# Optimization experiments

Hardware: AMD Instinct MI355X
Metric: run time of the kernel (lower is better)

## Reference

```python
import jax, jax.numpy as jnp
import numpy as np

E = 1024
B = 16384

def _ln(x, g, b, eps=1e-5):
    mu = jnp.mean(x, axis=-1, keepdims=True)
    var = jnp.mean(jnp.square(x - mu), axis=-1, keepdims=True)
    return (x - mu) * jax.lax.rsqrt(var + eps) * g + b

def setup_inputs() -> dict:
    key = jax.random.key(0)
    ks = jax.random.split(key, 16)
    s = 0.02
    return {
        'img_feat': jax.random.normal(ks[0], (B, E), jnp.float32),
        'txt_feat': jax.random.normal(ks[1], (B, E), jnp.float32),
        # MHA 1 (img queries txt): packed in_proj [3E, E] like torch
        'w_in1': jax.random.normal(ks[2], (3 * E, E), jnp.float32) * s,
        'b_in1': jnp.zeros((3 * E,), jnp.float32),
        'w_out1': jax.random.normal(ks[3], (E, E), jnp.float32) * s,
        'b_out1': jnp.zeros((E,), jnp.float32),
        # MHA 2 (txt queries img)
        'w_in2': jax.random.normal(ks[4], (3 * E, E), jnp.float32) * s,
        'b_in2': jnp.zeros((3 * E,), jnp.float32),
        'w_out2': jax.random.normal(ks[5], (E, E), jnp.float32) * s,
        'b_out2': jnp.zeros((E,), jnp.float32),
        # LayerNorms
        'g1': jnp.ones((E,), jnp.float32), 'be1': jnp.zeros((E,), jnp.float32),
        'g2': jnp.ones((E,), jnp.float32), 'be2': jnp.zeros((E,), jnp.float32),
        'g3': jnp.ones((E,), jnp.float32), 'be3': jnp.zeros((E,), jnp.float32),
        # FFN
        'w_ffn1': jax.random.normal(ks[6], (4 * E, E), jnp.float32) * s,
        'b_ffn1': jnp.zeros((4 * E,), jnp.float32),
        'w_ffn2': jax.random.normal(ks[7], (E, 4 * E), jnp.float32) * s,
        'b_ffn2': jnp.zeros((E,), jnp.float32),
    }

def _attn_seq1(q_in, kv_in, w_in, b_in, w_out, b_out):
    # seq_len==1 for both query and key: softmax over a single 1x1 score is
    # identically 1, so attention output == out_proj(v_proj(kv)). The q/k
    # projections cancel out exactly (same math as torch MHA in eval mode).
    wv = w_in[2 * E:]
    bv = b_in[2 * E:]
    v = kv_in @ wv.T + bv          # [B, E]
    return v @ w_out.T + b_out     # [B, E]

def reference(img_feat, txt_feat, w_in1, b_in1, w_out1, b_out1,
              w_in2, b_in2, w_out2, b_out2,
              g1, be1, g2, be2, g3, be3,
              w_ffn1, b_ffn1, w_ffn2, b_ffn2):
    img_att = _attn_seq1(img_feat, txt_feat, w_in1, b_in1, w_out1, b_out1)
    img = _ln(img_feat + img_att, g1, be1)
    txt_att = _attn_seq1(txt_feat, img, w_in2, b_in2, w_out2, b_out2)
    txt = _ln(txt_feat + txt_att, g2, be2)
    combined = img + txt
    h = jax.nn.gelu(combined @ w_ffn1.T + b_ffn1, approximate=False)
    ffn = h @ w_ffn2.T + b_ffn2
    return _ln(combined + ffn, g3, be3)
```

## Files before the change

kernel.cpp:

```cpp
#include <hip/hip_runtime.h>
#include <hip/hip_bf16.h>

typedef __bf16 bf16_t;
typedef __bf16 bf16x8 __attribute__((ext_vector_type(8)));
typedef __bf16 bf16x4 __attribute__((ext_vector_type(4)));
typedef float f32x4 __attribute__((ext_vector_type(4)));

static constexpr int E = 1024;
static constexpr int BROWS = 16384;
static constexpr size_t MB = 1ull << 20;

__device__ __forceinline__ float gelu_f(float x) {
  float t = __expf(-x * fmaf(0.0713548163f, x * x, 1.5957691216f));
  return x / (1.0f + t);
}

__global__ __launch_bounds__(256) void cvt_f32_bf16(const float* __restrict__ src,
                                                    bf16_t* __restrict__ dst, int n4) {
  int stride = gridDim.x * blockDim.x;
  for (int i = blockIdx.x * blockDim.x + threadIdx.x; i < n4; i += stride) {
    float4 v = reinterpret_cast<const float4*>(src)[i];
    bf16x4 o;
    o[0] = (bf16_t)v.x; o[1] = (bf16_t)v.y; o[2] = (bf16_t)v.z; o[3] = (bf16_t)v.w;
    reinterpret_cast<bf16x4*>(dst)[i] = o;
  }
}

__global__ __launch_bounds__(256) void cvt_transpose(const float* __restrict__ in,
                                                     bf16_t* __restrict__ out) {
  __shared__ float t[64][65];
  const int bx = blockIdx.x * 64, by = blockIdx.y * 64;
  const int tid = threadIdx.x;
  const int r = tid >> 2, c4 = (tid & 3) * 16;
#pragma unroll
  for (int j = 0; j < 4; ++j) {
    float4 v = *reinterpret_cast<const float4*>(&in[(long)(by + r) * E + bx + c4 + j * 4]);
    t[r][c4 + j * 4 + 0] = v.x;
    t[r][c4 + j * 4 + 1] = v.y;
    t[r][c4 + j * 4 + 2] = v.z;
    t[r][c4 + j * 4 + 3] = v.w;
  }
  __syncthreads();
#pragma unroll
  for (int j = 0; j < 16; j += 4) {
    bf16x4 o;
    o[0] = (bf16_t)t[c4 + j + 0][r];
    o[1] = (bf16_t)t[c4 + j + 1][r];
    o[2] = (bf16_t)t[c4 + j + 2][r];
    o[3] = (bf16_t)t[c4 + j + 3][r];
    *reinterpret_cast<bf16x4*>(&out[(long)(bx + r) * E + by + c4 + j]) = o;
  }
}

__global__ __launch_bounds__(256) void fuse_bias(const float* __restrict__ wo,
                                                 const float* __restrict__ bv,
                                                 const float* __restrict__ bo,
                                                 float* __restrict__ outb) {
  const int row = (blockIdx.x * 256 + threadIdx.x) >> 6;
  const int lane = threadIdx.x & 63;
  float s = 0.f;
  for (int k = lane; k < E; k += 64) s += wo[(long)row * E + k] * bv[k];
#pragma unroll
  for (int off = 32; off; off >>= 1) s += __shfl_down(s, off);
  if (lane == 0) outb[row] = s + bo[row];
}

__global__ __launch_bounds__(256) void gemm_bt_small(const bf16_t* __restrict__ A,
                                                     const bf16_t* __restrict__ Bw,
                                                     bf16_t* __restrict__ Cout, int K, int N,
                                                     int NBX) {
  const int nwg = gridDim.x;
  const int orig = blockIdx.x;
  const int q = nwg >> 3;
  const int wgid = (orig & 7) * q + (orig >> 3);
  const int bx = wgid % NBX;
  const int by = wgid / NBX;
  __shared__ bf16_t As[128 * 32];
  __shared__ bf16_t Bs[128 * 32];
  const int tid = threadIdx.x;
  const int lane = tid & 63;
  const int w = tid >> 6;
  const int wr = w >> 1, wc = w & 1;
  const long m0 = (long)by * 128;
  const long n0 = (long)bx * 128;
  const bf16_t* aSrc = A + (m0 + (tid >> 2)) * (long)K + (tid & 3) * 8;
  const bf16_t* bSrc = Bw + (n0 + (tid >> 2)) * (long)K + (tid & 3) * 8;
  f32x4 acc[4][4];
#pragma unroll
  for (int mi = 0; mi < 4; ++mi)
#pragma unroll
    for (int ni = 0; ni < 4; ++ni) acc[mi][ni] = {0.f, 0.f, 0.f, 0.f};
  const int nkt = K >> 5;
  for (int kt = 0; kt < nkt; ++kt) {
#pragma unroll
    for (int r = 0; r < 2; ++r) {
      __builtin_amdgcn_global_load_lds(
          (__attribute__((address_space(1))) void*)(aSrc + (long)r * 64 * K + kt * 32),
          (__attribute__((address_space(3))) void*)((char*)As + r * 4096 + w * 1024), 16, 0, 0);
      __builtin_amdgcn_global_load_lds(
          (__attribute__((address_space(1))) void*)(bSrc + (long)r * 64 * K + kt * 32),
          (__attribute__((address_space(3))) void*)((char*)Bs + r * 4096 + w * 1024), 16, 0, 0);
    }
    __syncthreads();
    bf16x8 af[4], bfv[4];
#pragma unroll
    for (int i = 0; i < 4; ++i) {
      af[i] = *reinterpret_cast<const bf16x8*>(
          &As[(wr * 64 + i * 16 + (lane & 15)) * 32 + (lane >> 4) * 8]);
      bfv[i] = *reinterpret_cast<const bf16x8*>(
          &Bs[(wc * 64 + i * 16 + (lane & 15)) * 32 + (lane >> 4) * 8]);
    }
#pragma unroll
    for (int mi = 0; mi < 4; ++mi)
#pragma unroll
      for (int ni = 0; ni < 4; ++ni)
        acc[mi][ni] = __builtin_amdgcn_mfma_f32_16x16x32_bf16(af[mi], bfv[ni], acc[mi][ni], 0, 0, 0);
    __syncthreads();
  }
  const long crow0 = m0 + wr * 64 + ((lane >> 4) * 4);
  const long ccol0 = n0 + wc * 64 + (lane & 15);
#pragma unroll
  for (int mi = 0; mi < 4; ++mi)
#pragma unroll
    for (int ni = 0; ni < 4; ++ni)
#pragma unroll
      for (int r = 0; r < 4; ++r)
        Cout[(crow0 + mi * 16 + r) * N + ccol0 + ni * 16] = (bf16_t)acc[mi][ni][r];
}

#define GLDS(gp, lp)                                                              \
  __builtin_amdgcn_global_load_lds((__attribute__((address_space(1))) void*)(gp), \
                                   (__attribute__((address_space(3))) void*)(lp), 16, 0, 0)

template <int ACT_GELU, int OUT_BF16>
__global__ __launch_bounds__(512, 4) void gemm128(const bf16_t* __restrict__ A,
                                                  const bf16_t* __restrict__ Bw,
                                                  const float* __restrict__ bias,
                                                  void* __restrict__ Cout, int K, int N,
                                                  int NBX) {
  __shared__ char smem[49152];
  const int nwg = gridDim.x;
  const int orig = blockIdx.x;
  const int q = nwg >> 3;
  const int wgid = (orig & 7) * q + (orig >> 3);
  const int bx = wgid % NBX;
  const int by = wgid / NBX;
  const long m0 = (long)by * 128;
  const long n0 = (long)bx * 256;

  const int tid = threadIdx.x;
  const int lane = tid & 63;
  const int w = tid >> 6;
  const int wr = w >> 2;
  const int wc = w & 3;

  const int sv = (lane & 7) ^ (lane >> 3);
  const int r2 = (lane >> 3) * 2 + (sv >> 2);
  const int kc = (sv & 3) * 8;
  const bf16_t* srcA = A + (m0 + w * 16 + r2) * (long)K + kc;
  const bf16_t* srcB0 = Bw + (n0 + w * 32 + r2) * (long)K + kc;
  const bf16_t* srcB1 = srcB0 + 16 * (long)K;

  const int laneoff =
      ((lane >> 1) & 7) * 128 +
      ((((((lane & 1) << 2) | (lane >> 4))) ^ ((lane >> 1) & 7)) << 4);
  const int wrOff = wr * 4096;
  const int wcOff = wc * 4096;

  f32x4 acc[4][4];
#pragma unroll
  for (int mi = 0; mi < 4; ++mi)
#pragma unroll
    for (int ni = 0; ni < 4; ++ni) acc[mi][ni] = {0.f, 0.f, 0.f, 0.f};

  GLDS(srcA, smem + w * 1024);
  GLDS(srcB0, smem + 8192 + w * 2048);
  GLDS(srcB1, smem + 8192 + w * 2048 + 1024);
  asm volatile("s_waitcnt vmcnt(0)" ::: "memory");
  asm volatile("s_barrier" ::: "memory");

  const int NS = K >> 5;
#pragma unroll 1
  for (int j = 0; j < NS; ++j) {
    const char* sb = smem + (j & 1) * 24576;
    if (j + 1 < NS) {
      char* sd = smem + ((j + 1) & 1) * 24576;
      const long t = (long)(j + 1) * 32;
      GLDS(srcA + t, sd + w * 1024);
      GLDS(srcB0 + t, sd + 8192 + w * 2048);
      GLDS(srcB1 + t, sd + 8192 + w * 2048 + 1024);
    }
    bf16x8 a[4], b[4];
#pragma unroll
    for (int i = 0; i < 4; ++i)
      a[i] = *reinterpret_cast<const bf16x8*>(sb + wrOff + i * 1024 + laneoff);
#pragma unroll
    for (int i = 0; i < 4; ++i)
      b[i] = *reinterpret_cast<const bf16x8*>(sb + 8192 + wcOff + i * 1024 + laneoff);
    __builtin_amdgcn_s_setprio(1);
#pragma unroll
    for (int mi = 0; mi < 4; ++mi)
#pragma unroll
      for (int ni = 0; ni < 4; ++ni)
        acc[mi][ni] = __builtin_amdgcn_mfma_f32_16x16x32_bf16(a[mi], b[ni], acc[mi][ni], 0, 0, 0);
    __builtin_amdgcn_s_setprio(0);
    asm volatile("s_waitcnt lgkmcnt(0)" ::: "memory");
    if (j + 1 < NS) asm volatile("s_waitcnt vmcnt(0)" ::: "memory");
    asm volatile("s_barrier" ::: "memory");
  }

  float bv[4];
#pragma unroll
  for (int ni = 0; ni < 4; ++ni) bv[ni] = bias[n0 + wc * 64 + ni * 16 + (lane & 15)];
  const long crow0 = m0 + wr * 64 + ((lane >> 4) * 4);
  const long ccol0 = n0 + wc * 64 + (lane & 15);
#pragma unroll
  for (int mi = 0; mi < 4; ++mi) {
#pragma unroll
    for (int ni = 0; ni < 4; ++ni) {
#pragma unroll
      for (int rr = 0; rr < 4; ++rr) {
        float v = acc[mi][ni][rr] + bv[ni];
        if (ACT_GELU) v = gelu_f(v);
        long idx = (crow0 + mi * 16 + rr) * N + ccol0 + ni * 16;
        if (OUT_BF16)
          ((bf16_t*)Cout)[idx] = (bf16_t)v;
        else
          ((float*)Cout)[idx] = v;
      }
    }
  }
}
#undef GLDS

template <int MODE>
__global__ __launch_bounds__(256) void ln_k(const float* __restrict__ Xf,
                                            const bf16_t* __restrict__ Xb,
                                            const float* __restrict__ Yf,
                                            const bf16_t* __restrict__ Yb,
                                            const float* __restrict__ gamma,
                                            const float* __restrict__ beta,
                                            const bf16_t* __restrict__ addB,
                                            float* __restrict__ outF,
                                            bf16_t* __restrict__ outB) {
  const int tid = threadIdx.x;
  const long base = (long)blockIdx.x * E;
  float4 s;
  if (MODE < 2) {
    float4 xv = reinterpret_cast<const float4*>(Xf + base)[tid];
    bf16x4 yv = reinterpret_cast<const bf16x4*>(Yb + base)[tid];
    s.x = xv.x + (float)yv[0]; s.y = xv.y + (float)yv[1];
    s.z = xv.z + (float)yv[2]; s.w = xv.w + (float)yv[3];
  } else {
    bf16x4 xv = reinterpret_cast<const bf16x4*>(Xb + base)[tid];
    float4 yv = reinterpret_cast<const float4*>(Yf + base)[tid];
    s.x = (float)xv[0] + yv.x; s.y = (float)xv[1] + yv.y;
    s.z = (float)xv[2] + yv.z; s.w = (float)xv[3] + yv.w;
  }
  float sum = s.x + s.y + s.z + s.w;
  float sq = s.x * s.x + s.y * s.y + s.z * s.z + s.w * s.w;
#pragma unroll
  for (int off = 32; off > 0; off >>= 1) {
    sum += __shfl_down(sum, off);
    sq += __shfl_down(sq, off);
  }
  __shared__ float red[2][4];
  const int w = tid >> 6;
  if ((tid & 63) == 0) { red[0][w] = sum; red[1][w] = sq; }
  __syncthreads();
  float tot = red[0][0] + red[0][1] + red[0][2] + red[0][3];
  float tsq = red[1][0] + red[1][1] + red[1][2] + red[1][3];
  const float mu = tot * (1.0f / E);
  const float var = tsq * (1.0f / E) - mu * mu;
  const float rs = rsqrtf(var + 1e-5f);
  float4 gv = reinterpret_cast<const float4*>(gamma)[tid];
  float4 bvv = reinterpret_cast<const float4*>(beta)[tid];
  float4 o;
  o.x = (s.x - mu) * rs * gv.x + bvv.x;
  o.y = (s.y - mu) * rs * gv.y + bvv.y;
  o.z = (s.z - mu) * rs * gv.z + bvv.z;
  o.w = (s.w - mu) * rs * gv.w + bvv.w;
  if (MODE == 1) {
    bf16x4 av = reinterpret_cast<const bf16x4*>(addB + base)[tid];
    o.x += (float)av[0]; o.y += (float)av[1]; o.z += (float)av[2]; o.w += (float)av[3];
  }
  if (MODE == 2) {
    reinterpret_cast<float4*>(outF + base)[tid] = o;
  } else {
    bf16x4 ob;
    ob[0] = (bf16_t)o.x; ob[1] = (bf16_t)o.y; ob[2] = (bf16_t)o.z; ob[3] = (bf16_t)o.w;
    reinterpret_cast<bf16x4*>(outB + base)[tid] = ob;
  }
}

extern "C" void kernel_launch(void* const* d_in, const int* in_sizes, int n_in, void* d_out,
                              int out_size, void* d_ws, size_t ws_size, hipStream_t stream) {
  const float* img_feat = (const float*)d_in[0];
  const float* txt_feat = (const float*)d_in[1];
  const float* w_in1 = (const float*)d_in[2];
  const float* b_in1 = (const float*)d_in[3];
  const float* w_out1 = (const float*)d_in[4];
  const float* b_out1 = (const float*)d_in[5];
  const float* w_in2 = (const float*)d_in[6];
  const float* b_in2 = (const float*)d_in[7];
  const float* w_out2 = (const float*)d_in[8];
  const float* b_out2 = (const float*)d_in[9];
  const float* g1 = (const float*)d_in[10];
  const float* be1 = (const float*)d_in[11];
  const float* g2 = (const float*)d_in[12];
  const float* be2 = (const float*)d_in[13];
  const float* g3 = (const float*)d_in[14];
  const float* be3 = (const float*)d_in[15];
  const float* w_ffn1 = (const float*)d_in[16];
  const float* b_ffn1 = (const float*)d_in[17];
  const float* w_ffn2 = (const float*)d_in[18];
  const float* b_ffn2 = (const float*)d_in[19];

  if (ws_size < 184 * MB) return;
  char* ws = (char*)d_ws;
  bf16_t* TXTB = (bf16_t*)(ws + 0 * MB);
  bf16_t* ATT = (bf16_t*)(ws + 32 * MB);
  bf16_t* IMGB = (bf16_t*)(ws + 64 * MB);
  bf16_t* H = (bf16_t*)(ws + 0 * MB);
  bf16_t* COMB = (bf16_t*)(ws + 128 * MB);
  bf16_t* T0 = (bf16_t*)(ws + 160 * MB);
  bf16_t* T1 = (bf16_t*)(ws + 162 * MB);
  bf16_t* Wc1 = (bf16_t*)(ws + 164 * MB);
  bf16_t* Wc2 = (bf16_t*)(ws + 166 * MB);
  bf16_t* wf1b = (bf16_t*)(ws + 168 * MB);
  bf16_t* wf2b = (bf16_t*)(ws + 176 * MB);
  float* bias1 = (float*)d_out;
  float* bias2 = bias1 + E;

  dim3 blk(256);
  dim3 blk512(512);
  cvt_f32_bf16<<<dim3(2048), blk, 0, stream>>>(txt_feat, TXTB, BROWS * E / 4);
  cvt_f32_bf16<<<dim3(1024), blk, 0, stream>>>(w_ffn1, wf1b, 4 * E * E / 4);
  cvt_f32_bf16<<<dim3(1024), blk, 0, stream>>>(w_ffn2, wf2b, 4 * E * E / 4);

  cvt_transpose<<<dim3(16, 16), blk, 0, stream>>>(w_in1 + 2 * E * E, T0);
  cvt_f32_bf16<<<dim3(512), blk, 0, stream>>>(w_out1, T1, E * E / 4);
  gemm_bt_small<<<dim3(64), blk, 0, stream>>>(T1, T0, Wc1, E, E, 8);
  fuse_bias<<<dim3(256), blk, 0, stream>>>(w_out1, b_in1 + 2 * E, b_out1, bias1);

  cvt_transpose<<<dim3(16, 16), blk, 0, stream>>>(w_in2 + 2 * E * E, T0);
  cvt_f32_bf16<<<dim3(512), blk, 0, stream>>>(w_out2, T1, E * E / 4);
  gemm_bt_small<<<dim3(64), blk, 0, stream>>>(T1, T0, Wc2, E, E, 8);
  fuse_bias<<<dim3(256), blk, 0, stream>>>(w_out2, b_in2 + 2 * E, b_out2, bias2);

  gemm128<0, 1><<<dim3(512), blk512, 0, stream>>>(TXTB, Wc1, bias1, ATT, E, E, 4);
  ln_k<0><<<dim3(BROWS), blk, 0, stream>>>(img_feat, nullptr, nullptr, ATT, g1, be1, nullptr,
                                           nullptr, IMGB);
  gemm128<0, 1><<<dim3(512), blk512, 0, stream>>>(IMGB, Wc2, bias2, ATT, E, E, 4);
  ln_k<1><<<dim3(BROWS), blk, 0, stream>>>(txt_feat, nullptr, nullptr, ATT, g2, be2, IMGB,
                                           nullptr, COMB);
  gemm128<1, 1><<<dim3(2048), blk512, 0, stream>>>(COMB, wf1b, b_ffn1, H, E, 4 * E, 16);
  gemm128<0, 0><<<dim3(512), blk512, 0, stream>>>(H, wf2b, b_ffn2, d_out, 4 * E, E, 4);
  ln_k<2><<<dim3(BROWS), blk, 0, stream>>>(nullptr, COMB, (float*)d_out, nullptr, g3, be3,
                                           nullptr, (float*)d_out, nullptr);
}
```

Measured before the change: 568.1 us.

## Triple-buffer GEMM LDS pipeline and batch weight-prep kernels into fewer launches

The main GEMM goes from double to triple buffering: shared memory grows to 72 KB, two K-stages are prefetched ahead, and each iteration waits on vmcnt(3) instead of draining all loads. Separately, the paired weight-preparation kernels (conversions, transposes, small weight-fusion GEMMs, bias fusion) for the two attention blocks and the FFN weights are merged into single launches to cut launch overhead. The larger LDS footprint may reduce occupancy below the four blocks per CU the launch bounds request.

```diff
diff --git a/kernel.cpp b/kernel.cpp
--- a/kernel.cpp
+++ b/kernel.cpp
@@ -26,8 +26,28 @@
   }
 }
 
-__global__ __launch_bounds__(256) void cvt_transpose(const float* __restrict__ in,
-                                                     bf16_t* __restrict__ out) {
+__global__ __launch_bounds__(256) void cvt2_f32_bf16(const float* __restrict__ s1,
+                                                     bf16_t* __restrict__ d1,
+                                                     const float* __restrict__ s2,
+                                                     bf16_t* __restrict__ d2, int n4) {
+  int stride = gridDim.x * blockDim.x;
+  for (int i = blockIdx.x * blockDim.x + threadIdx.x; i < 2 * n4; i += stride) {
+    const float* src = (i < n4) ? s1 : s2;
+    bf16_t* dst = (i < n4) ? d1 : d2;
+    int k = (i < n4) ? i : i - n4;
+    float4 v = reinterpret_cast<const float4*>(src)[k];
+    bf16x4 o;
+    o[0] = (bf16_t)v.x; o[1] = (bf16_t)v.y; o[2] = (bf16_t)v.z; o[3] = (bf16_t)v.w;
+    reinterpret_cast<bf16x4*>(dst)[k] = o;
+  }
+}
+
+__global__ __launch_bounds__(256) void cvt_transpose2(const float* __restrict__ in1,
+                                                      bf16_t* __restrict__ out1,
+                                                      const float* __restrict__ in2,
+                                                      bf16_t* __restrict__ out2) {
+  const float* in = blockIdx.z ? in2 : in1;
+  bf16_t* out = blockIdx.z ? out2 : out1;
   __shared__ float t[64][65];
   const int bx = blockIdx.x * 64, by = blockIdx.y * 64;
   const int tid = threadIdx.x;
@@ -52,12 +72,21 @@
   }
 }
 
-__global__ __launch_bounds__(256) void fuse_bias(const float* __restrict__ wo,
-                                                 const float* __restrict__ bv,
-                                                 const float* __restrict__ bo,
-                                                 float* __restrict__ outb) {
-  const int row = (blockIdx.x * 256 + threadIdx.x) >> 6;
+__global__ __launch_bounds__(256) void fuse_bias2(const float* __restrict__ wo1,
+                                                  const float* __restrict__ bv1,
+                                                  const float* __restrict__ bo1,
+                                                  float* __restrict__ out1,
+                                                  const float* __restrict__ wo2,
+                                                  const float* __restrict__ bv2,
+                                                  const float* __restrict__ bo2,
+                                                  float* __restrict__ out2) {
+  const int gr = (blockIdx.x * 256 + threadIdx.x) >> 6;
   const int lane = threadIdx.x & 63;
+  const int row = gr & 1023;
+  const float* wo = (gr < 1024) ? wo1 : wo2;
+  const float* bv = (gr < 1024) ? bv1 : bv2;
+  const float* bo = (gr < 1024) ? bo1 : bo2;
+  float* outb = (gr < 1024) ? out1 : out2;
   float s = 0.f;
   for (int k = lane; k < E; k += 64) s += wo[(long)row * E + k] * bv[k];
 #pragma unroll
@@ -65,16 +94,21 @@
   if (lane == 0) outb[row] = s + bo[row];
 }
 
-__global__ __launch_bounds__(256) void gemm_bt_small(const bf16_t* __restrict__ A,
-                                                     const bf16_t* __restrict__ Bw,
-                                                     bf16_t* __restrict__ Cout, int K, int N,
-                                                     int NBX) {
-  const int nwg = gridDim.x;
+__global__ __launch_bounds__(256) void gemm_small2(const bf16_t* __restrict__ A1,
+                                                   const bf16_t* __restrict__ B1,
+                                                   bf16_t* __restrict__ C1,
+                                                   const bf16_t* __restrict__ A2,
+                                                   const bf16_t* __restrict__ B2,
+                                                   bf16_t* __restrict__ C2) {
+  const int K = 1024, N = 1024;
   const int orig = blockIdx.x;
-  const int q = nwg >> 3;
-  const int wgid = (orig & 7) * q + (orig >> 3);
-  const int bx = wgid % NBX;
-  const int by = wgid / NBX;
+  const int wgid = (orig & 7) * 16 + (orig >> 3);
+  const int bx = wgid & 7;
+  const int byy = wgid >> 3;
+  const bf16_t* A = (byy < 8) ? A1 : A2;
+  const bf16_t* Bw = (byy < 8) ? B1 : B2;
+  bf16_t* Cout = (byy < 8) ? C1 : C2;
+  const int by = byy & 7;
   __shared__ bf16_t As[128 * 32];
   __shared__ bf16_t Bs[128 * 32];
   const int tid = threadIdx.x;
@@ -138,7 +172,7 @@
                                                   const float* __restrict__ bias,
                                                   void* __restrict__ Cout, int K, int N,
                                                   int NBX) {
-  __shared__ char smem[49152];
+  __shared__ char smem[73728];
   const int nwg = gridDim.x;
   const int orig = blockIdx.x;
   const int q = nwg >> 3;
@@ -161,6 +195,15 @@
   const bf16_t* srcB0 = Bw + (n0 + w * 32 + r2) * (long)K + kc;
   const bf16_t* srcB1 = srcB0 + 16 * (long)K;
 
+#define STAGE(s, t)                                    \
+  {                                                    \
+    char* sd = smem + (s) * 24576;                     \
+    const long tt = (long)(t) * 32;                    \
+    GLDS(srcA + tt, sd + w * 1024);                    \
+    GLDS(srcB0 + tt, sd + 8192 + w * 2048);            \
+    GLDS(srcB1 + tt, sd + 8192 + w * 2048 + 1024);     \
+  }
+
   const int laneoff =
       ((lane >> 1) & 7) * 128 +
       ((((((lane & 1) << 2) | (lane >> 4))) ^ ((lane >> 1) & 7)) << 4);
@@ -173,22 +216,20 @@
 #pragma unroll
     for (int ni = 0; ni < 4; ++ni) acc[mi][ni] = {0.f, 0.f, 0.f, 0.f};
 
-  GLDS(srcA, smem + w * 1024);
-  GLDS(srcB0, smem + 8192 + w * 2048);
-  GLDS(srcB1, smem + 8192 + w * 2048 + 1024);
-  asm volatile("s_waitcnt vmcnt(0)" ::: "memory");
+  STAGE(0, 0);
+  STAGE(1, 1);
+  asm volatile("s_waitcnt vmcnt(3)" ::: "memory");
   asm volatile("s_barrier" ::: "memory");
 
   const int NS = K >> 5;
+  int cur = 0;
 #pragma unroll 1
   for (int j = 0; j < NS; ++j) {
-    const char* sb = smem + (j & 1) * 24576;
-    if (j + 1 < NS) {
-      char* sd = smem + ((j + 1) & 1) * 24576;
-      const long t = (long)(j + 1) * 32;
-      GLDS(srcA + t, sd + w * 1024);
-      GLDS(srcB0 + t, sd + 8192 + w * 2048);
-      GLDS(srcB1 + t, sd + 8192 + w * 2048 + 1024);
+    const char* sb = smem + cur * 24576;
+    if (j + 2 < NS) {
+      int nx = cur + 2;
+      if (nx >= 3) nx -= 3;
+      STAGE(nx, j + 2);
     }
     bf16x8 a[4], b[4];
 #pragma unroll
@@ -204,9 +245,15 @@
       for (int ni = 0; ni < 4; ++ni)
         acc[mi][ni] = __builtin_amdgcn_mfma_f32_16x16x32_bf16(a[mi], b[ni], acc[mi][ni], 0, 0, 0);
     __builtin_amdgcn_s_setprio(0);
-    asm volatile("s_waitcnt lgkmcnt(0)" ::: "memory");
-    if (j + 1 < NS) asm volatile("s_waitcnt vmcnt(0)" ::: "memory");
-    asm volatile("s_barrier" ::: "memory");
+    if (j + 1 < NS) {
+      asm volatile("s_waitcnt lgkmcnt(0)" ::: "memory");
+      if (j + 2 < NS)
+        asm volatile("s_waitcnt vmcnt(3)" ::: "memory");
+      else
+        asm volatile("s_waitcnt vmcnt(0)" ::: "memory");
+      asm volatile("s_barrier" ::: "memory");
+    }
+    cur = (cur + 1 == 3) ? 0 : cur + 1;
   }
 
   float bv[4];
@@ -230,6 +277,7 @@
       }
     }
   }
+#undef STAGE
 }
 #undef GLDS
 
@@ -321,32 +369,30 @@
   bf16_t* TXTB = (bf16_t*)(ws + 0 * MB);
   bf16_t* ATT = (bf16_t*)(ws + 32 * MB);
   bf16_t* IMGB = (bf16_t*)(ws + 64 * MB);
+  bf16_t* T0a = (bf16_t*)(ws + 64 * MB);
+  bf16_t* T0b = (bf16_t*)(ws + 66 * MB);
+  bf16_t* T1a = (bf16_t*)(ws + 68 * MB);
+  bf16_t* T1b = (bf16_t*)(ws + 70 * MB);
   bf16_t* H = (bf16_t*)(ws + 0 * MB);
   bf16_t* COMB = (bf16_t*)(ws + 128 * MB);
-  bf16_t* T0 = (bf16_t*)(ws + 160 * MB);
-  bf16_t* T1 = (bf16_t*)(ws + 162 * MB);
-  bf16_t* Wc1 = (bf16_t*)(ws + 164 * MB);
-  bf16_t* Wc2 = (bf16_t*)(ws + 166 * MB);
-  bf16_t* wf1b = (bf16_t*)(ws + 168 * MB);
-  bf16_t* wf2b = (bf16_t*)(ws + 176 * MB);
+  bf16_t* Wc1 = (bf16_t*)(ws + 160 * MB);
+  bf16_t* Wc2 = (bf16_t*)(ws + 162 * MB);
+  bf16_t* wf1b = (bf16_t*)(ws + 164 * MB);
+  bf16_t* wf2b = (bf16_t*)(ws + 172 * MB);
   float* bias1 = (float*)d_out;
   float* bias2 = bias1 + E;
 
   dim3 blk(256);
   dim3 blk512(512);
   cvt_f32_bf16<<<dim3(2048), blk, 0, stream>>>(txt_feat, TXTB, BROWS * E / 4);
-  cvt_f32_bf16<<<dim3(1024), blk, 0, stream>>>(w_ffn1, wf1b, 4 * E * E / 4);
-  cvt_f32_bf16<<<dim3(1024), blk, 0, stream>>>(w_ffn2, wf2b, 4 * E * E / 4);
-
-  cvt_transpose<<<dim3(16, 16), blk, 0, stream>>>(w_in1 + 2 * E * E, T0);
-  cvt_f32_bf16<<<dim3(512), blk, 0, stream>>>(w_out1, T1, E * E / 4);
-  gemm_bt_small<<<dim3(64), blk, 0, stream>>>(T1, T0, Wc1, E, E, 8);
-  fuse_bias<<<dim3(256), blk, 0, stream>>>(w_out1, b_in1 + 2 * E, b_out1, bias1);
-
-  cvt_transpose<<<dim3(16, 16), blk, 0, stream>>>(w_in2 + 2 * E * E, T0);
-  cvt_f32_bf16<<<dim3(512), blk, 0, stream>>>(w_out2, T1, E * E / 4);
-  gemm_bt_small<<<dim3(64), blk, 0, stream>>>(T1, T0, Wc2, E, E, 8);
-  fuse_bias<<<dim3(256), blk, 0, stream>>>(w_out2, b_in2 + 2 * E, b_out2, bias2);
+  cvt2_f32_bf16<<<dim3(2048), blk, 0, stream>>>(w_ffn1, wf1b, w_ffn2, wf2b, 4 * E * E / 4);
+
+  cvt_transpose2<<<dim3(16, 16, 2), blk, 0, stream>>>(w_in1 + 2 * E * E, T0a,
+                                                      w_in2 + 2 * E * E, T0b);
+  cvt2_f32_bf16<<<dim3(1024), blk, 0, stream>>>(w_out1, T1a, w_out2, T1b, E * E / 4);
+  gemm_small2<<<dim3(128), blk, 0, stream>>>(T1a, T0a, Wc1, T1b, T0b, Wc2);
+  fuse_bias2<<<dim3(512), blk, 0, stream>>>(w_out1, b_in1 + 2 * E, b_out1, bias1,
+                                            w_out2, b_in2 + 2 * E, b_out2, bias2);
 
   gemm128<0, 1><<<dim3(512), blk512, 0, stream>>>(TXTB, Wc1, bias1, ATT, E, E, 4);
   ln_k<0><<<dim3(BROWS), blk, 0, stream>>>(img_feat, nullptr, nullptr, ATT, g1, be1, nullptr,
```

Measured after the change: 528.6 us. -7.0%, faster.
